# Performance work log

Hardware: AMD Instinct MI355X
Metric: run time of the kernel (lower is better)

## Reference

```python
import jax, jax.numpy as jnp
import numpy as np

N_NODES = 50000
N_EDGES = 800000
N_GRAPHS = 256
HID = 64           # hidden_channels
H, C = 2, 64       # GAT heads, per-head channels
D2 = H * C         # 128 = hidden_channels * heads
BN_EPS = 1e-5


def setup_inputs() -> dict:
    key = jax.random.key(0)
    ks = iter(jax.random.split(key, 64))

    def p(shape, scale=0.05):
        return (jax.random.normal(next(ks), shape, dtype=jnp.float32) * scale)

    inp = {}
    inp["metadata"] = jax.random.normal(next(ks), (N_NODES, 4), dtype=jnp.float32)
    inp["waveform_features"] = jax.random.normal(next(ks), (N_NODES, 64), dtype=jnp.float32)
    inp["edge_index"] = jax.random.randint(next(ks), (2, N_EDGES), 0, N_NODES, dtype=jnp.int64)
    inp["batch"] = jnp.sort(jax.random.randint(next(ks), (N_NODES,), 0, N_GRAPHS, dtype=jnp.int64))

    # encoders / combiner
    inp["meta_w"] = p((4, HID // 2)); inp["meta_b"] = p((HID // 2,))
    inp["wave_w"] = p((64, HID // 2)); inp["wave_b"] = p((HID // 2,))
    inp["comb_w"] = p((HID, HID));     inp["comb_b"] = p((HID,))

    # GAT layers: layer 0 maps HID->H*C, layers 1,2 map D2->H*C
    inp["gat_w0"] = p((HID, D2)); inp["gat_as0"] = p((H, C)); inp["gat_ad0"] = p((H, C)); inp["gat_b0"] = p((D2,))
    inp["gat_w1"] = p((D2, D2));  inp["gat_as1"] = p((H, C)); inp["gat_ad1"] = p((H, C)); inp["gat_b1"] = p((D2,))
    inp["gat_w2"] = p((D2, D2));  inp["gat_as2"] = p((H, C)); inp["gat_ad2"] = p((H, C)); inp["gat_b2"] = p((D2,))

    # batch norms (eval mode: running stats), stacked over 3 layers
    inp["bn_gamma"] = jnp.ones((3, D2), jnp.float32) + p((3, D2))
    inp["bn_beta"] = p((3, D2))
    inp["bn_mean"] = p((3, D2))
    inp["bn_var"] = jax.random.uniform(next(ks), (3, D2), jnp.float32, 0.5, 1.5)

    # predictors
    inp["lat_w1"] = p((D2, HID)); inp["lat_b1"] = p((HID,))
    inp["lat_w2"] = p((HID, 1));  inp["lat_b2"] = p((1,))
    inp["lon_w1"] = p((D2, HID)); inp["lon_b1"] = p((HID,))
    inp["lon_w2"] = p((HID, 1));  inp["lon_b2"] = p((1,))
    return inp


def gat_conv(x, src, dst, n, W, a_src, a_dst, b):
    """PyG-style GATConv, heads=H concat, leaky_relu slope 0.2, self-loops already in src/dst."""
    h = (x @ W).reshape(n, H, C)                          # [N,H,C]
    s = jnp.einsum('nhc,hc->nh', h, a_src)                # alpha_src [N,H]
    d = jnp.einsum('nhc,hc->nh', h, a_dst)                # alpha_dst [N,H]
    e = jax.nn.leaky_relu(s[src] + d[dst], 0.2)           # [E,H]
    m = jax.ops.segment_max(e, dst, num_segments=n)       # per-dst softmax (segment)
    ex = jnp.exp(e - m[dst])
    denom = jax.ops.segment_sum(ex, dst, num_segments=n)
    alpha = ex / (denom[dst] + 1e-16)                     # [E,H]
    out = jax.ops.segment_sum(h[src] * alpha[:, :, None], dst, num_segments=n)  # [N,H,C]
    return out.reshape(n, H * C) + b


def reference(metadata, waveform_features, edge_index, batch,
              meta_w, meta_b, wave_w, wave_b, comb_w, comb_b,
              gat_w0, gat_as0, gat_ad0, gat_b0,
              gat_w1, gat_as1, gat_ad1, gat_b1,
              gat_w2, gat_as2, gat_ad2, gat_b2,
              bn_gamma, bn_beta, bn_mean, bn_var,
              lat_w1, lat_b1, lat_w2, lat_b2,
              lon_w1, lon_b1, lon_w2, lon_b2):
    n = metadata.shape[0]
    me = jax.nn.relu(metadata @ meta_w + meta_b)
    we = jax.nn.relu(waveform_features @ wave_w + wave_b)
    x = jnp.concatenate([me, we], axis=1)                 # [N, HID]
    x = jax.nn.relu(x @ comb_w + comb_b)

    loops = jnp.arange(n, dtype=edge_index.dtype)         # GATConv adds self-loops
    src = jnp.concatenate([edge_index[0], loops])
    dst = jnp.concatenate([edge_index[1], loops])

    gat_params = [(gat_w0, gat_as0, gat_ad0, gat_b0),
                  (gat_w1, gat_as1, gat_ad1, gat_b1),
                  (gat_w2, gat_as2, gat_ad2, gat_b2)]
    for i in range(3):
        x_res = x if i > 0 else None
        x = gat_conv(x, src, dst, n, *gat_params[i])
        x = (x - bn_mean[i]) * (bn_gamma[i] / jnp.sqrt(bn_var[i] + BN_EPS)) + bn_beta[i]
        if x_res is not None and x.shape == x_res.shape:
            x = x + x_res
        x = jax.nn.relu(x)                                # dropout inactive (eval)

    # global_mean_pool over graphs
    sums = jax.ops.segment_sum(x, batch, num_segments=N_GRAPHS)
    cnt = jax.ops.segment_sum(jnp.ones((n, 1), x.dtype), batch, num_segments=N_GRAPHS)
    xg = sums / jnp.maximum(cnt, 1.0)                     # [B, 128]

    lat = jax.nn.relu(xg @ lat_w1 + lat_b1) @ lat_w2 + lat_b2
    lon = jax.nn.relu(xg @ lon_w1 + lon_b1) @ lon_w2 + lon_b2
    return lat, lon
```

## Files before the change

kernel.cpp:

```cpp
#include <hip/hip_runtime.h>
#include <hip/hip_bf16.h>
#include <stdint.h>

#define NN 50000
#define NNP 50048
#define NE 800000
#define ET 850000
#define NG 256
#define CAP 128
#define NB 392
#define BCAP 3072
#define EB 4096
#define NEB ((ET + EB - 1) / EB)

typedef __hip_bfloat16 bf16;
typedef __attribute__((ext_vector_type(8))) short short8;
typedef __attribute__((ext_vector_type(4))) float floatx4;

__device__ __forceinline__ float b2f(bf16 v) { return __bfloat162float(v); }
__device__ __forceinline__ float lrelu(float x) { return x > 0.f ? x : 0.2f * x; }
__device__ __forceinline__ short f2b(float f) {
    unsigned u = __float_as_uint(f);
    unsigned r = (u + 0x7FFFu + ((u >> 16) & 1u)) >> 16;
    return (short)r;
}
__device__ __forceinline__ float sh2f(short s) { return __uint_as_float(((unsigned)(unsigned short)s) << 16); }
__device__ __forceinline__ float blo(unsigned u) { return __uint_as_float(u << 16); }
__device__ __forceinline__ float bhi(unsigned u) { return __uint_as_float(u & 0xFFFF0000u); }
__device__ __forceinline__ unsigned pck(float a, float b) {
    return ((unsigned)(unsigned short)f2b(a)) | (((unsigned)(unsigned short)f2b(b)) << 16);
}
__device__ __forceinline__ float wred_sum(float v) {
    for (int o = 32; o > 0; o >>= 1) v += __shfl_xor(v, o, 64);
    return v;
}
__device__ __forceinline__ int ld_int(const void* p, int i, bool i64) {
    return i64 ? (int)((const long long*)p)[i] : ((const int*)p)[i];
}
__device__ __forceinline__ float ldf(const void* p, int i, bool fp32) {
    return fp32 ? ((const float*)p)[i] : b2f(((const bf16*)p)[i]);
}

__global__ void detect_kernel(const unsigned int* __restrict__ meta_words,
                              const unsigned int* __restrict__ ei_words,
                              int* __restrict__ flags, int* __restrict__ bcur) {
    __shared__ int insane, odd_nonzero;
    for (int k = threadIdx.x; k < NB; k += 256) bcur[k] = 0;
    if (threadIdx.x == 0) { insane = 0; odd_nonzero = 0; }
    __syncthreads();
    int cnt = 0;
    for (int k = 0; k < 8; k++) {
        unsigned int w = meta_words[threadIdx.x * 8 + k];
        int elo = (int)(((w & 0xFFFFu) >> 7) & 0xFF);
        int ehi = (int)(((w >> 16) >> 7) & 0xFF);
        if (elo >= 0x8D) cnt++;
        if (ehi >= 0x8D) cnt++;
    }
    if (cnt) atomicAdd(&insane, cnt);
    if (ei_words[threadIdx.x * 2 + 1] != 0u) atomicAdd(&odd_nonzero, 1);
    __syncthreads();
    if (threadIdx.x == 0) {
        flags[0] = (insane >= 4) ? 1 : 0;
        flags[1] = (odd_nonzero == 0) ? 1 : 0;
    }
}

struct PrepArgs {
    const void* src[32];
    int len[32];
    int dst_off[32];
    int blk_base[33];
    int cvtBlks, wtBlks, wfBlks;
    const void* w0; const void* w1; const void* w2;
    const void* ww; const void* wc;
    const void* wf_src;
    const void* gb0; const void* gb1; const void* gb2;
    const void* bng; const void* bnb; const void* bnm; const void* bnv;
};

__global__ void prep_kernel(PrepArgs a, float* __restrict__ cf,
                            short* __restrict__ wtall, short* __restrict__ wavewT,
                            short* __restrict__ combwT,
                            short* __restrict__ wfhi, short* __restrict__ wflo,
                            float* __restrict__ bnscl, float* __restrict__ bnsft,
                            const int* __restrict__ flags) {
    int b = blockIdx.x;
    bool fp32f = flags[0] != 0;
    if (b < a.cvtBlks) {
        int ai = 0;
        while (b >= a.blk_base[ai + 1]) ai++;
        int base = (b - a.blk_base[ai]) * 1024 + threadIdx.x;
        const float* sf = (const float*)a.src[ai];
        const bf16* sh = (const bf16*)a.src[ai];
        float* d = cf + a.dst_off[ai];
        int len = a.len[ai];
        #pragma unroll
        for (int u = 0; u < 4; u++) {
            int i = base + u * 256;
            if (i < len) d[i] = fp32f ? sf[i] : b2f(sh[i]);
        }
        return;
    }
    b -= a.cvtBlks;
    if (b < a.wtBlks) {
        int idx = b * 256 + threadIdx.x;
        const void* src; short* dst; int K, N, loc;
        if (idx < 8192)        { src = a.w0; dst = wtall;          K = 64;  N = 128; loc = idx; }
        else if (idx < 24576)  { src = a.w1; dst = wtall + 8192;   K = 128; N = 128; loc = idx - 8192; }
        else if (idx < 40960)  { src = a.w2; dst = wtall + 24576;  K = 128; N = 128; loc = idx - 24576; }
        else if (idx < 43008)  { src = a.ww; dst = wavewT;         K = 64;  N = 32;  loc = idx - 40960; }
        else if (idx < 47104)  { src = a.wc; dst = combwT;         K = 64;  N = 64;  loc = idx - 43008; }
        else return;
        int nch = loc / K, k = loc % K;
        int si = k * N + nch;
        dst[loc] = fp32f ? f2b(((const float*)src)[si]) : ((const short*)src)[si];
        return;
    }
    b -= a.wtBlks;
    if (b < a.wfBlks) {
        int idx = b * 256 + threadIdx.x;
        int i8 = idx * 8;
        if (i8 >= NNP * 64) return;
        short8 h = {0, 0, 0, 0, 0, 0, 0, 0};
        if (fp32f) {
            short8 l = {0, 0, 0, 0, 0, 0, 0, 0};
            if (i8 < NN * 64) {
                const float* sf = (const float*)a.wf_src + i8;
                #pragma unroll
                for (int k = 0; k < 8; k++) {
                    float v = sf[k];
                    short hh = f2b(v);
                    h[k] = hh;
                    l[k] = f2b(v - sh2f(hh));
                }
            }
            *(short8*)(wfhi + i8) = h;
            *(short8*)(wflo + i8) = l;
        } else {
            if (i8 < NN * 64) h = *(const short8*)((const short*)a.wf_src + i8);
            *(short8*)(wfhi + i8) = h;
        }
        return;
    }
    b -= a.wfBlks;
    int idx = b * 256 + threadIdx.x;
    if (idx >= 384) return;
    int l = idx >> 7, c = idx & 127;
    const void* biasp = (l == 0) ? a.gb0 : (l == 1) ? a.gb1 : a.gb2;
    float bias = ldf(biasp, c, fp32f);
    float g  = ldf(a.bng, l * 128 + c, fp32f);
    float be = ldf(a.bnb, l * 128 + c, fp32f);
    float mu = ldf(a.bnm, l * 128 + c, fp32f);
    float va = ldf(a.bnv, l * 128 + c, fp32f);
    float sc = g * rsqrtf(va + 1e-5f);
    bnscl[l * 128 + c] = sc;
    bnsft[l * 128 + c] = (bias - mu) * sc + be;
}

__global__ __launch_bounds__(256) void encode_mfma_kernel(
        const float* __restrict__ meta, const float* __restrict__ meta_w,
        const float* __restrict__ meta_b,
        const short* __restrict__ wfhi, const short* __restrict__ wflo,
        const short* __restrict__ wavewT, const float* __restrict__ wave_b,
        const short* __restrict__ combwT, const float* __restrict__ comb_b,
        short* __restrict__ xout, const int* __restrict__ flags) {
    __shared__ short xc_hi[64][72];
    __shared__ short xc_lo[64][72];
    int t = threadIdx.x;
    int wave = t >> 6, lane = t & 63;
    int m16 = lane & 15, quad = lane >> 4;
    int nblk = blockIdx.x * 64;
    bool fp32f = flags[0] != 0;

    #pragma unroll
    for (int u = 0; u < 8; u++) {
        int idx = u * 256 + t;
        int node_l = idx >> 5, ch = idx & 31;
        int node = nblk + node_l;
        float acc = meta_b[ch];
        if (node < NN) {
            #pragma unroll
            for (int k = 0; k < 4; k++)
                acc += meta[node * 4 + k] * meta_w[k * 32 + ch];
        }
        float v = fmaxf(acc, 0.f);
        short hh = f2b(v);
        xc_hi[node_l][ch] = hh;
        xc_lo[node_l][ch] = f2b(v - sh2f(hh));
    }

    int row0 = nblk + wave * 16;
    const short* pah = wfhi + (size_t)(row0 + m16) * 64 + quad * 8;
    const short* pal = wflo + (size_t)(row0 + m16) * 64 + quad * 8;
    floatx4 wacc[2];
    wacc[0] = (floatx4)(0.f); wacc[1] = (floatx4)(0.f);
    #pragma unroll
    for (int ks = 0; ks < 64; ks += 32) {
        short8 ah = *(const short8*)(pah + ks);
        #pragma unroll
        for (int c = 0; c < 2; c++) {
            short8 b = *(const short8*)(wavewT + (c * 16 + m16) * 64 + ks + quad * 8);
            wacc[c] = __builtin_amdgcn_mfma_f32_16x16x32_bf16(ah, b, wacc[c], 0, 0, 0);
        }
        if (fp32f) {
            short8 al = *(const short8*)(pal + ks);
            #pragma unroll
            for (int c = 0; c < 2; c++) {
                short8 b = *(const short8*)(wavewT + (c * 16 + m16) * 64 + ks + quad * 8);
                wacc[c] = __builtin_amdgcn_mfma_f32_16x16x32_bf16(al, b, wacc[c], 0, 0, 0);
            }
        }
    }
    #pragma unroll
    for (int c = 0; c < 2; c++) {
        float bb = wave_b[c * 16 + m16];
        #pragma unroll
        for (int r = 0; r < 4; r++) {
            int node_l = wave * 16 + quad * 4 + r;
            int ch = 32 + c * 16 + m16;
            float v = fmaxf(wacc[c][r] + bb, 0.f);
            short hh = f2b(v);
            xc_hi[node_l][ch] = hh;
            xc_lo[node_l][ch] = f2b(v - sh2f(hh));
        }
    }
    __syncthreads();

    floatx4 acc2[4];
    #pragma unroll
    for (int c = 0; c < 4; c++) acc2[c] = (floatx4)(0.f);
    #pragma unroll
    for (int ks = 0; ks < 64; ks += 32) {
        short8 ah = *(const short8*)&xc_hi[wave * 16 + m16][ks + quad * 8];
        short8 al = *(const short8*)&xc_lo[wave * 16 + m16][ks + quad * 8];
        #pragma unroll
        for (int c = 0; c < 4; c++) {
            short8 b = *(const short8*)(combwT + (c * 16 + m16) * 64 + ks + quad * 8);
            acc2[c] = __builtin_amdgcn_mfma_f32_16x16x32_bf16(ah, b, acc2[c], 0, 0, 0);
            acc2[c] = __builtin_amdgcn_mfma_f32_16x16x32_bf16(al, b, acc2[c], 0, 0, 0);
        }
    }
    #pragma unroll
    for (int c = 0; c < 4; c++) {
        int ch = c * 16 + m16;
        float bb = comb_b[ch];
        #pragma unroll
        for (int r = 0; r < 4; r++) {
            int node = nblk + wave * 16 + quad * 4 + r;
            float v = fmaxf(acc2[c][r] + bb, 0.f);
            xout[(size_t)node * 64 + ch] = f2b(v);
        }
    }
}

__global__ void bucket_scatter_kernel(const void* __restrict__ ei, const int* __restrict__ flags,
                                      int* __restrict__ bcur, uint2* __restrict__ bkt) {
    __shared__ int lh[NB];
    __shared__ int lbase[NB];
    int t = threadIdx.x;
    bool i64 = flags[1] != 0;
    for (int k = t; k < NB; k += 256) lh[k] = 0;
    __syncthreads();
    int base = blockIdx.x * EB;
    #pragma unroll 4
    for (int u = 0; u < EB / 256; u++) {
        int i = base + u * 256 + t;
        if (i < ET) {
            int dst = (i < NE) ? ld_int(ei, NE + i, i64) : (i - NE);
            atomicAdd(&lh[dst >> 7], 1);
        }
    }
    __syncthreads();
    for (int k = t; k < NB; k += 256) {
        int c = lh[k];
        lbase[k] = c ? atomicAdd(&bcur[k], c) : 0;
        lh[k] = 0;
    }
    __syncthreads();
    #pragma unroll 4
    for (int u = 0; u < EB / 256; u++) {
        int i = base + u * 256 + t;
        if (i < ET) {
            int src, dst;
            if (i < NE) { src = ld_int(ei, i, i64); dst = ld_int(ei, NE + i, i64); }
            else        { src = i - NE; dst = i - NE; }
            int b = dst >> 7;
            int pos = lbase[b] + atomicAdd(&lh[b], 1);
            if (pos < BCAP) bkt[(size_t)b * BCAP + pos] = make_uint2((unsigned)src, (unsigned)dst);
        }
    }
}

__global__ void bucket_finalize_kernel(const uint2* __restrict__ bkt,
                                       const int* __restrict__ bcnt,
                                       int* __restrict__ offb, int* __restrict__ dega,
                                       int* __restrict__ csr) {
    __shared__ int hist[128];
    __shared__ int cur[128];
    int b = blockIdx.x;
    int t = threadIdx.x;
    int e0 = b * BCAP;
    int cnt = min(bcnt[b], BCAP);
    if (t < 128) hist[t] = 0;
    __syncthreads();
    for (int i = t; i < cnt; i += 256)
        atomicAdd(&hist[bkt[e0 + i].y & 127], 1);
    __syncthreads();
    int v = (t < 128) ? hist[t] : 0;
    if (t < 128) cur[t] = v;
    __syncthreads();
    for (int o = 1; o < 128; o <<= 1) {
        int x = (t < 128 && t >= o) ? cur[t - o] : 0;
        __syncthreads();
        if (t < 128) cur[t] += x;
        __syncthreads();
    }
    if (t < 128) {
        int ex = e0 + cur[t] - v;
        int node = b * 128 + t;
        if (node < NN) { offb[node] = ex; dega[node] = v; }
        cur[t] = ex;
    }
    __syncthreads();
    for (int i = t; i < cnt; i += 256) {
        uint2 e = bkt[e0 + i];
        int pos = atomicAdd(&cur[e.y & 127], 1);
        csr[pos] = (int)e.x;
    }
}

__global__ __launch_bounds__(256) void gemm_mfma_kernel(
        const short* __restrict__ x, const short* __restrict__ wt,
        const float* __restrict__ a_s, const float* __restrict__ a_d,
        short* __restrict__ h, float* __restrict__ s, float* __restrict__ d,
        int K, int n) {
    int wave = threadIdx.x >> 6;
    int lane = threadIdx.x & 63;
    int row0 = (blockIdx.x * 4 + wave) * 16;
    int m16 = lane & 15;
    int quad = lane >> 4;
    int kq = quad * 8;

    const short* pa = x + (size_t)(row0 + m16) * K + kq;

    floatx4 acc[8];
    #pragma unroll
    for (int c = 0; c < 8; c++) acc[c] = (floatx4)(0.f);

    for (int ks = 0; ks < K; ks += 32) {
        short8 av = *(const short8*)(pa + ks);
        #pragma unroll
        for (int c = 0; c < 8; c++) {
            short8 b = *(const short8*)(wt + (size_t)(c * 16 + m16) * K + ks + kq);
            acc[c] = __builtin_amdgcn_mfma_f32_16x16x32_bf16(av, b, acc[c], 0, 0, 0);
        }
    }

    #pragma unroll
    for (int c = 0; c < 8; c++) {
        #pragma unroll
        for (int r = 0; r < 4; r++) {
            int node = row0 + quad * 4 + r;
            if (node < n) h[(size_t)node * 128 + c * 16 + m16] = f2b(acc[c][r]);
        }
    }

    float sp[2][4] = {{0, 0, 0, 0}, {0, 0, 0, 0}};
    float dp[2][4] = {{0, 0, 0, 0}, {0, 0, 0, 0}};
    #pragma unroll
    for (int c = 0; c < 8; c++) {
        float as_ = a_s[c * 16 + m16];
        float ad_ = a_d[c * 16 + m16];
        int hh = c >> 2;
        #pragma unroll
        for (int r = 0; r < 4; r++) {
            sp[hh][r] += acc[c][r] * as_;
            dp[hh][r] += acc[c][r] * ad_;
        }
    }
    #pragma unroll
    for (int o = 1; o < 16; o <<= 1) {
        #pragma unroll
        for (int hh = 0; hh < 2; hh++)
            #pragma unroll
            for (int r = 0; r < 4; r++) {
                sp[hh][r] += __shfl_xor(sp[hh][r], o, 64);
                dp[hh][r] += __shfl_xor(dp[hh][r], o, 64);
            }
    }
    if (m16 == 0) {
        #pragma unroll
        for (int r = 0; r < 4; r++) {
            int node = row0 + quad * 4 + r;
            if (node < n) {
                s[node * 2 + 0] = sp[0][r];
                s[node * 2 + 1] = sp[1][r];
                d[node * 2 + 0] = dp[0][r];
                d[node * 2 + 1] = dp[1][r];
            }
        }
    }
}

__global__ __launch_bounds__(256) void gat_aggregate_kernel(
        const unsigned* __restrict__ hp, const float* __restrict__ sv,
        const float* __restrict__ dv, const int* __restrict__ offb,
        const int* __restrict__ dega, const int* __restrict__ csr,
        const float* __restrict__ scl, const float* __restrict__ sft,
        const unsigned* __restrict__ res, unsigned* __restrict__ out, int n) {
    __shared__ float4 er[8][CAP];
    int slot = threadIdx.x >> 5;
    int lane32 = threadIdx.x & 31;
    int node = blockIdx.x * 8 + slot;
    bool ok = node < n;
    int begin = 0, deg = 0;
    float d0 = 0.f, d1 = 0.f;
    if (ok) {
        begin = offb[node]; deg = dega[node];
        d0 = dv[node * 2 + 0]; d1 = dv[node * 2 + 1];
    }
    bool fits = deg <= CAP;
    int degp = (deg + 7) & ~7;
    float inv0 = 0.f, inv1 = 0.f;

    if (ok && fits) {
        int sids[4]; float e0[4], e1[4];
        #pragma unroll
        for (int k = 0; k < 4; k++) {
            int li = k * 32 + lane32;
            sids[k] = (li < deg) ? csr[begin + li] : -1;
        }
        #pragma unroll
        for (int k = 0; k < 4; k++) {
            if (sids[k] >= 0) {
                float2 sp = *(const float2*)(sv + 2 * sids[k]);
                e0[k] = lrelu(sp.x + d0); e1[k] = lrelu(sp.y + d1);
            } else { e0[k] = -3e38f; e1[k] = -3e38f; }
        }
        float m0 = fmaxf(fmaxf(e0[0], e0[1]), fmaxf(e0[2], e0[3]));
        float m1 = fmaxf(fmaxf(e1[0], e1[1]), fmaxf(e1[2], e1[3]));
        #pragma unroll
        for (int o = 1; o < 32; o <<= 1) {
            m0 = fmaxf(m0, __shfl_xor(m0, o, 64));
            m1 = fmaxf(m1, __shfl_xor(m1, o, 64));
        }
        float z0 = 0.f, z1 = 0.f;
        #pragma unroll
        for (int k = 0; k < 4; k++) {
            if (sids[k] >= 0) {
                float x0 = __expf(e0[k] - m0), x1 = __expf(e1[k] - m1);
                z0 += x0; z1 += x1;
                er[slot][k * 32 + lane32] = make_float4(__int_as_float(sids[k]), x0, x1, 0.f);
            }
        }
        #pragma unroll
        for (int o = 1; o < 32; o <<= 1) {
            z0 += __shfl_xor(z0, o, 64);
            z1 += __shfl_xor(z1, o, 64);
        }
        if (lane32 < degp - deg)
            er[slot][deg + lane32] = make_float4(__int_as_float(0), 0.f, 0.f, 0.f);
        inv0 = 1.f / (z0 + 1e-16f);
        inv1 = 1.f / (z1 + 1e-16f);
    }
    __syncthreads();
    if (!ok) return;

    if (fits) {
        int ll = lane32 & 15;
        int grp = lane32 >> 4;
        int hsel = (ll >= 8) ? 1 : 0;
        const uint4* hp4 = (const uint4*)hp;
        float a0 = 0, a1 = 0, a2 = 0, a3 = 0, a4 = 0, a5 = 0, a6 = 0, a7 = 0;
        for (int i = 0; i < degp; i += 8) {
            int e = i + grp * 4;
            float4 r0 = er[slot][e], r1 = er[slot][e + 1], r2 = er[slot][e + 2], r3 = er[slot][e + 3];
            uint4 u0 = hp4[(size_t)__float_as_int(r0.x) * 16 + ll];
            uint4 u1 = hp4[(size_t)__float_as_int(r1.x) * 16 + ll];
            uint4 u2 = hp4[(size_t)__float_as_int(r2.x) * 16 + ll];
            uint4 u3 = hp4[(size_t)__float_as_int(r3.x) * 16 + ll];
            float al0 = hsel ? r0.z : r0.y;
            float al1 = hsel ? r1.z : r1.y;
            float al2 = hsel ? r2.z : r2.y;
            float al3 = hsel ? r3.z : r3.y;
            a0 += al0 * blo(u0.x) + al1 * blo(u1.x) + al2 * blo(u2.x) + al3 * blo(u3.x);
            a1 += al0 * bhi(u0.x) + al1 * bhi(u1.x) + al2 * bhi(u2.x) + al3 * bhi(u3.x);
            a2 += al0 * blo(u0.y) + al1 * blo(u1.y) + al2 * blo(u2.y) + al3 * blo(u3.y);
            a3 += al0 * bhi(u0.y) + al1 * bhi(u1.y) + al2 * bhi(u2.y) + al3 * bhi(u3.y);
            a4 += al0 * blo(u0.z) + al1 * blo(u1.z) + al2 * blo(u2.z) + al3 * blo(u3.z);
            a5 += al0 * bhi(u0.z) + al1 * bhi(u1.z) + al2 * bhi(u2.z) + al3 * bhi(u3.z);
            a6 += al0 * blo(u0.w) + al1 * blo(u1.w) + al2 * blo(u2.w) + al3 * blo(u3.w);
            a7 += al0 * bhi(u0.w) + al1 * bhi(u1.w) + al2 * bhi(u2.w) + al3 * bhi(u3.w);
        }
        a0 += __shfl_xor(a0, 16, 64); a1 += __shfl_xor(a1, 16, 64);
        a2 += __shfl_xor(a2, 16, 64); a3 += __shfl_xor(a3, 16, 64);
        a4 += __shfl_xor(a4, 16, 64); a5 += __shfl_xor(a5, 16, 64);
        a6 += __shfl_xor(a6, 16, 64); a7 += __shfl_xor(a7, 16, 64);
        float inv = hsel ? inv1 : inv0;
        a0 *= inv; a1 *= inv; a2 *= inv; a3 *= inv;
        a4 *= inv; a5 *= inv; a6 *= inv; a7 *= inv;

        float4 sc0 = ((const float4*)scl)[2 * ll], sc1 = ((const float4*)scl)[2 * ll + 1];
        float4 sh0 = ((const float4*)sft)[2 * ll], sh1 = ((const float4*)sft)[2 * ll + 1];
        float v0 = a0 * sc0.x + sh0.x;
        float v1 = a1 * sc0.y + sh0.y;
        float v2 = a2 * sc0.z + sh0.z;
        float v3 = a3 * sc0.w + sh0.w;
        float v4 = a4 * sc1.x + sh1.x;
        float v5 = a5 * sc1.y + sh1.y;
        float v6 = a6 * sc1.z + sh1.z;
        float v7 = a7 * sc1.w + sh1.w;
        if (res) {
            uint4 r = ((const uint4*)res)[(size_t)node * 16 + ll];
            v0 += blo(r.x); v1 += bhi(r.x); v2 += blo(r.y); v3 += bhi(r.y);
            v4 += blo(r.z); v5 += bhi(r.z); v6 += blo(r.w); v7 += bhi(r.w);
        }
        v0 = fmaxf(v0, 0.f); v1 = fmaxf(v1, 0.f); v2 = fmaxf(v2, 0.f); v3 = fmaxf(v3, 0.f);
        v4 = fmaxf(v4, 0.f); v5 = fmaxf(v5, 0.f); v6 = fmaxf(v6, 0.f); v7 = fmaxf(v7, 0.f);
        if (grp == 0) {
            ((uint4*)out)[(size_t)node * 16 + ll] =
                make_uint4(pck(v0, v1), pck(v2, v3), pck(v4, v5), pck(v6, v7));
        }
    } else {
        float mm0 = -3e38f, mm1 = -3e38f;
        for (int i = lane32; i < deg; i += 32) {
            int sc = csr[begin + i];
            float2 sp = *(const float2*)(sv + 2 * sc);
            mm0 = fmaxf(mm0, lrelu(sp.x + d0));
            mm1 = fmaxf(mm1, lrelu(sp.y + d1));
        }
        #pragma unroll
        for (int o = 1; o < 32; o <<= 1) {
            mm0 = fmaxf(mm0, __shfl_xor(mm0, o, 64));
            mm1 = fmaxf(mm1, __shfl_xor(mm1, o, 64));
        }
        float z0 = 0.f, z1 = 0.f;
        for (int i = lane32; i < deg; i += 32) {
            int sc = csr[begin + i];
            float2 sp = *(const float2*)(sv + 2 * sc);
            z0 += __expf(lrelu(sp.x + d0) - mm0);
            z1 += __expf(lrelu(sp.y + d1) - mm1);
        }
        #pragma unroll
        for (int o = 1; o < 32; o <<= 1) {
            z0 += __shfl_xor(z0, o, 64);
            z1 += __shfl_xor(z1, o, 64);
        }
        float i0_ = 1.f / (z0 + 1e-16f), i1_ = 1.f / (z1 + 1e-16f);
        bool head0 = lane32 < 16;
        float b0 = 0.f, b1 = 0.f, b2 = 0.f, b3 = 0.f;
        for (int i = 0; i < deg; i++) {
            int sc = csr[begin + i];
            float2 sp = *(const float2*)(sv + 2 * sc);
            float a = head0 ? __expf(lrelu(sp.x + d0) - mm0) * i0_
                            : __expf(lrelu(sp.y + d1) - mm1) * i1_;
            uint2 u = *(const uint2*)(hp + (size_t)sc * 64 + lane32 * 2);
            b0 += a * blo(u.x); b1 += a * bhi(u.x);
            b2 += a * blo(u.y); b3 += a * bhi(u.y);
        }
        float4 sc4 = ((const float4*)scl)[lane32];
        float4 sh4 = ((const float4*)sft)[lane32];
        float v0 = b0 * sc4.x + sh4.x;
        float v1 = b1 * sc4.y + sh4.y;
        float v2 = b2 * sc4.z + sh4.z;
        float v3 = b3 * sc4.w + sh4.w;
        if (res) {
            uint2 r = ((const uint2*)res)[(size_t)node * 32 + lane32];
            v0 += blo(r.x); v1 += bhi(r.x); v2 += blo(r.y); v3 += bhi(r.y);
        }
        v0 = fmaxf(v0, 0.f); v1 = fmaxf(v1, 0.f);
        v2 = fmaxf(v2, 0.f); v3 = fmaxf(v3, 0.f);
        ((uint2*)out)[(size_t)node * 32 + lane32] = make_uint2(pck(v0, v1), pck(v2, v3));
    }
}

__global__ void poolhead_kernel(const unsigned* __restrict__ x, const void* __restrict__ batch,
                                const float* __restrict__ w1a, const float* __restrict__ b1a,
                                const float* __restrict__ w2a, const float* __restrict__ b2a,
                                const float* __restrict__ w1o, const float* __restrict__ b1o,
                                const float* __restrict__ w2o, const float* __restrict__ b2o,
                                const int* __restrict__ flags, void* __restrict__ out) {
    __shared__ float part[4][128];
    __shared__ float xs[128];
    __shared__ int bounds[2];
    int g = blockIdx.x;
    int tid = threadIdx.x;
    bool i64 = flags[1] != 0;
    if (tid < 2) {
        int target = g + tid;
        int lo = 0, hi = NN;
        while (lo < hi) {
            int mid = (lo + hi) >> 1;
            if (ld_int(batch, mid, i64) < target) lo = mid + 1; else hi = mid;
        }
        bounds[tid] = lo;
    }
    __syncthreads();
    int s0 = bounds[0], e0 = bounds[1];
    int wv = tid >> 6, lane = tid & 63;
    float a0 = 0.f, a1 = 0.f;
    for (int node = s0 + wv; node < e0; node += 4) {
        unsigned u = x[(size_t)node * 64 + lane];
        a0 += blo(u);
        a1 += bhi(u);
    }
    part[wv][2 * lane] = a0;
    part[wv][2 * lane + 1] = a1;
    __syncthreads();
    if (tid < 128) {
        float t0 = part[0][tid] + part[1][tid] + part[2][tid] + part[3][tid];
        xs[tid] = t0 / fmaxf((float)(e0 - s0), 1.f);
    }
    __syncthreads();
    if (wv < 2) {
        const float* w1 = wv ? w1o : w1a;
        const float* b1 = wv ? b1o : b1a;
        const float* w2 = wv ? w2o : w2a;
        const float* b2 = wv ? b2o : b2a;
        float acc = b1[lane];
        for (int c = 0; c < 128; c++)
            acc += xs[c] * w1[c * 64 + lane];
        acc = fmaxf(acc, 0.f);
        float contrib = wred_sum(acc * w2[lane]);
        if (lane == 0) {
            float r = contrib + b2[0];
            if (flags[0]) ((float*)out)[wv * NG + g] = r;
            else          ((bf16*)out)[wv * NG + g] = __float2bfloat16(r);
        }
    }
}

extern "C" void kernel_launch(void* const* d_in, const int* in_sizes, int n_in,
                              void* d_out, int out_size, void* d_ws, size_t ws_size,
                              hipStream_t stream) {
    static const int fidx[32] = {0,1, 4,5,6,7,8,9, 10,11,12,13, 14,15,16,17,
                                 18,19,20,21, 22,23,24,25, 26,27,28,29, 30,31,32,33};
    static const int flen[32] = {200000, 3200000, 128, 32, 2048, 32, 4096, 64,
                                 8192, 128, 128, 128, 16384, 128, 128, 128,
                                 16384, 128, 128, 128, 384, 384, 384, 384,
                                 8192, 64, 64, 1, 8192, 64, 64, 1};
    PrepArgs pa;
    int O[32];
    int tot = 0, blk = 0;
    for (int i = 0; i < 32; i++) {
        bool skip = (i == 1) || (i == 4) || (i == 6) || (i == 8) || (i == 12) || (i == 16) ||
                    (i == 11) || (i == 15) || (i == 19) ||
                    (i == 20) || (i == 21) || (i == 22) || (i == 23);
        int cl = skip ? 0 : flen[i];
        pa.src[i] = d_in[fidx[i]];
        pa.len[i] = cl;
        O[i] = tot;
        pa.dst_off[i] = tot;
        pa.blk_base[i] = blk;
        tot += (flen[i] + 63) & ~63;
        blk += (cl + 1023) / 1024;
    }
    pa.blk_base[32] = blk;
    pa.cvtBlks = blk;
    pa.wtBlks = 184;
    pa.wfBlks = NNP * 64 / 8 / 256;
    pa.w0 = d_in[10]; pa.w1 = d_in[14]; pa.w2 = d_in[18];
    pa.ww = d_in[6];  pa.wc = d_in[8];
    pa.wf_src = d_in[1];
    pa.gb0 = d_in[13]; pa.gb1 = d_in[17]; pa.gb2 = d_in[21];
    pa.bng = d_in[22]; pa.bnb = d_in[23]; pa.bnm = d_in[24]; pa.bnv = d_in[25];
    int prepGrid = pa.cvtBlks + pa.wtBlks + pa.wfBlks + 2;

    char* w = (char*)d_ws;
    auto alloc = [&](size_t bytes) -> char* {
        char* p = w;
        w += (bytes + 255) & ~(size_t)255;
        return p;
    };
    int*   flags  = (int*)alloc(256);
    float* cf     = (float*)alloc((size_t)tot * 4);
    short* wfhi   = (short*)alloc((size_t)NNP * 64 * 2);
    short* wflo   = (short*)alloc((size_t)NNP * 64 * 2);
    short* x0     = (short*)alloc((size_t)NNP * 64 * 2);
    short* xA     = (short*)alloc((size_t)NNP * 128 * 2);
    short* xB     = (short*)alloc((size_t)NNP * 128 * 2);
    short* h      = (short*)alloc((size_t)NNP * 128 * 2);
    float* sA     = (float*)alloc((size_t)NN * 2 * 4);
    float* dA     = (float*)alloc((size_t)NN * 2 * 4);
    int*   offb   = (int*)alloc((size_t)NN * 4);
    int*   dega   = (int*)alloc((size_t)NN * 4);
    int*   csr    = (int*)alloc((size_t)NB * BCAP * 4);
    int*   bcur   = (int*)alloc((size_t)NB * 4);
    uint2* bkt    = (uint2*)alloc((size_t)NB * BCAP * 8);
    float* bnscl  = (float*)alloc(384 * 4);
    float* bnsft  = (float*)alloc(384 * 4);
    short* wtall  = (short*)alloc((size_t)40960 * 2);
    short* wavewT = (short*)alloc((size_t)2048 * 2);
    short* combwT = (short*)alloc((size_t)4096 * 2);
    short* wt0 = wtall, *wt1 = wtall + 8192, *wt2 = wtall + 24576;

    detect_kernel<<<1, 256, 0, stream>>>((const unsigned int*)d_in[0],
                                         (const unsigned int*)d_in[2], flags, bcur);
    prep_kernel<<<prepGrid, 256, 0, stream>>>(pa, cf, wtall, wavewT, combwT,
                                              wfhi, wflo, bnscl, bnsft, flags);
    encode_mfma_kernel<<<NNP / 64, 256, 0, stream>>>(cf + O[0], cf + O[2], cf + O[3],
                                                     wfhi, wflo, wavewT, cf + O[5],
                                                     combwT, cf + O[7], x0, flags);
    bucket_scatter_kernel<<<NEB, 256, 0, stream>>>(d_in[2], flags, bcur, bkt);
    bucket_finalize_kernel<<<NB, 256, 0, stream>>>(bkt, bcur, offb, dega, csr);

    int gblk = NNP / 64;
    gemm_mfma_kernel<<<gblk, 256, 0, stream>>>(x0, wt0, cf + O[9], cf + O[10],
                                               h, sA, dA, 64, NN);
    gat_aggregate_kernel<<<(NN + 7) / 8, 256, 0, stream>>>(
        (const unsigned*)h, sA, dA, offb, dega, csr,
        bnscl, bnsft, nullptr, (unsigned*)xA, NN);
    gemm_mfma_kernel<<<gblk, 256, 0, stream>>>(xA, wt1, cf + O[13], cf + O[14],
                                               h, sA, dA, 128, NN);
    gat_aggregate_kernel<<<(NN + 7) / 8, 256, 0, stream>>>(
        (const unsigned*)h, sA, dA, offb, dega, csr,
        bnscl + 128, bnsft + 128, (const unsigned*)xA, (unsigned*)xB, NN);
    gemm_mfma_kernel<<<gblk, 256, 0, stream>>>(xB, wt2, cf + O[17], cf + O[18],
                                               h, sA, dA, 128, NN);
    gat_aggregate_kernel<<<(NN + 7) / 8, 256, 0, stream>>>(
        (const unsigned*)h, sA, dA, offb, dega, csr,
        bnscl + 256, bnsft + 256, (const unsigned*)xB, (unsigned*)xA, NN);

    poolhead_kernel<<<NG, 256, 0, stream>>>((const unsigned*)xA, d_in[3],
                                            cf + O[24], cf + O[25], cf + O[26], cf + O[27],
                                            cf + O[28], cf + O[29], cf + O[30], cf + O[31],
                                            flags, d_out);
}
```

Baseline: 365.4 us.

## Store GAT projected features in fp32 and skip bf16 waveform copy

The intermediate h produced by the GEMM is now stored as fp32 instead of bf16. The aggregation kernels read fp32 float4 pairs in the gather instead of unpacking bf16, which doubles the gather traffic over about 850k edges per layer. The aim is to improve accuracy and cut conversion ALU work, at the cost of more memory bandwidth. Separately, when the input is already bf16, the prep step no longer copies the waveform features and the encoder reads the raw input directly, with a row clamp replacing the old padding.

```diff
diff --git a/kernel.cpp b/kernel.cpp
--- a/kernel.cpp
+++ b/kernel.cpp
@@ -118,28 +118,24 @@
     }
     b -= a.wtBlks;
     if (b < a.wfBlks) {
+        if (!fp32f) return;
         int idx = b * 256 + threadIdx.x;
         int i8 = idx * 8;
         if (i8 >= NNP * 64) return;
         short8 h = {0, 0, 0, 0, 0, 0, 0, 0};
-        if (fp32f) {
-            short8 l = {0, 0, 0, 0, 0, 0, 0, 0};
-            if (i8 < NN * 64) {
-                const float* sf = (const float*)a.wf_src + i8;
-                #pragma unroll
-                for (int k = 0; k < 8; k++) {
-                    float v = sf[k];
-                    short hh = f2b(v);
-                    h[k] = hh;
-                    l[k] = f2b(v - sh2f(hh));
-                }
+        short8 l = {0, 0, 0, 0, 0, 0, 0, 0};
+        if (i8 < NN * 64) {
+            const float* sf = (const float*)a.wf_src + i8;
+            #pragma unroll
+            for (int k = 0; k < 8; k++) {
+                float v = sf[k];
+                short hh = f2b(v);
+                h[k] = hh;
+                l[k] = f2b(v - sh2f(hh));
             }
-            *(short8*)(wfhi + i8) = h;
-            *(short8*)(wflo + i8) = l;
-        } else {
-            if (i8 < NN * 64) h = *(const short8*)((const short*)a.wf_src + i8);
-            *(short8*)(wfhi + i8) = h;
-        }
+        }
+        *(short8*)(wfhi + i8) = h;
+        *(short8*)(wflo + i8) = l;
         return;
     }
     b -= a.wfBlks;
@@ -161,6 +157,7 @@
         const float* __restrict__ meta, const float* __restrict__ meta_w,
         const float* __restrict__ meta_b,
         const short* __restrict__ wfhi, const short* __restrict__ wflo,
+        const short* __restrict__ wf_raw,
         const short* __restrict__ wavewT, const float* __restrict__ wave_b,
         const short* __restrict__ combwT, const float* __restrict__ comb_b,
         short* __restrict__ xout, const int* __restrict__ flags) {
@@ -189,9 +186,11 @@
         xc_lo[node_l][ch] = f2b(v - sh2f(hh));
     }
 
-    int row0 = nblk + wave * 16;
-    const short* pah = wfhi + (size_t)(row0 + m16) * 64 + quad * 8;
-    const short* pal = wflo + (size_t)(row0 + m16) * 64 + quad * 8;
+    int row = nblk + wave * 16 + m16;
+    if (row >= NN) row = NN - 1;
+    const short* wbase = fp32f ? wfhi : wf_raw;
+    const short* pah = wbase + (size_t)row * 64 + quad * 8;
+    const short* pal = wflo + (size_t)row * 64 + quad * 8;
     floatx4 wacc[2];
     wacc[0] = (floatx4)(0.f); wacc[1] = (floatx4)(0.f);
     #pragma unroll
@@ -332,7 +331,7 @@
 __global__ __launch_bounds__(256) void gemm_mfma_kernel(
         const short* __restrict__ x, const short* __restrict__ wt,
         const float* __restrict__ a_s, const float* __restrict__ a_d,
-        short* __restrict__ h, float* __restrict__ s, float* __restrict__ d,
+        float* __restrict__ h, float* __restrict__ s, float* __restrict__ d,
         int K, int n) {
     int wave = threadIdx.x >> 6;
     int lane = threadIdx.x & 63;
@@ -361,7 +360,7 @@
         #pragma unroll
         for (int r = 0; r < 4; r++) {
             int node = row0 + quad * 4 + r;
-            if (node < n) h[(size_t)node * 128 + c * 16 + m16] = f2b(acc[c][r]);
+            if (node < n) h[(size_t)node * 128 + c * 16 + m16] = acc[c][r];
         }
     }
 
@@ -403,7 +402,7 @@
 }
 
 __global__ __launch_bounds__(256) void gat_aggregate_kernel(
-        const unsigned* __restrict__ hp, const float* __restrict__ sv,
+        const float* __restrict__ hpf, const float* __restrict__ sv,
         const float* __restrict__ dv, const int* __restrict__ offb,
         const int* __restrict__ dega, const int* __restrict__ csr,
         const float* __restrict__ scl, const float* __restrict__ sft,
@@ -470,27 +469,31 @@
         int ll = lane32 & 15;
         int grp = lane32 >> 4;
         int hsel = (ll >= 8) ? 1 : 0;
-        const uint4* hp4 = (const uint4*)hp;
+        const float4* hp4 = (const float4*)hpf;
         float a0 = 0, a1 = 0, a2 = 0, a3 = 0, a4 = 0, a5 = 0, a6 = 0, a7 = 0;
         for (int i = 0; i < degp; i += 8) {
             int e = i + grp * 4;
             float4 r0 = er[slot][e], r1 = er[slot][e + 1], r2 = er[slot][e + 2], r3 = er[slot][e + 3];
-            uint4 u0 = hp4[(size_t)__float_as_int(r0.x) * 16 + ll];
-            uint4 u1 = hp4[(size_t)__float_as_int(r1.x) * 16 + ll];
-            uint4 u2 = hp4[(size_t)__float_as_int(r2.x) * 16 + ll];
-            uint4 u3 = hp4[(size_t)__float_as_int(r3.x) * 16 + ll];
+            int b0 = __float_as_int(r0.x) * 32 + ll * 2;
+            int b1 = __float_as_int(r1.x) * 32 + ll * 2;
+            int b2 = __float_as_int(r2.x) * 32 + ll * 2;
+            int b3 = __float_as_int(r3.x) * 32 + ll * 2;
+            float4 u0a = hp4[b0], u0b = hp4[b0 + 1];
+            float4 u1a = hp4[b1], u1b = hp4[b1 + 1];
+            float4 u2a = hp4[b2], u2b = hp4[b2 + 1];
+            float4 u3a = hp4[b3], u3b = hp4[b3 + 1];
             float al0 = hsel ? r0.z : r0.y;
             float al1 = hsel ? r1.z : r1.y;
             float al2 = hsel ? r2.z : r2.y;
             float al3 = hsel ? r3.z : r3.y;
-            a0 += al0 * blo(u0.x) + al1 * blo(u1.x) + al2 * blo(u2.x) + al3 * blo(u3.x);
-            a1 += al0 * bhi(u0.x) + al1 * bhi(u1.x) + al2 * bhi(u2.x) + al3 * bhi(u3.x);
-            a2 += al0 * blo(u0.y) + al1 * blo(u1.y) + al2 * blo(u2.y) + al3 * blo(u3.y);
-            a3 += al0 * bhi(u0.y) + al1 * bhi(u1.y) + al2 * bhi(u2.y) + al3 * bhi(u3.y);
-            a4 += al0 * blo(u0.z) + al1 * blo(u1.z) + al2 * blo(u2.z) + al3 * blo(u3.z);
-            a5 += al0 * bhi(u0.z) + al1 * bhi(u1.z) + al2 * bhi(u2.z) + al3 * bhi(u3.z);
-            a6 += al0 * blo(u0.w) + al1 * blo(u1.w) + al2 * blo(u2.w) + al3 * blo(u3.w);
-            a7 += al0 * bhi(u0.w) + al1 * bhi(u1.w) + al2 * bhi(u2.w) + al3 * bhi(u3.w);
+            a0 += al0 * u0a.x + al1 * u1a.x + al2 * u2a.x + al3 * u3a.x;
+            a1 += al0 * u0a.y + al1 * u1a.y + al2 * u2a.y + al3 * u3a.y;
+            a2 += al0 * u0a.z + al1 * u1a.z + al2 * u2a.z + al3 * u3a.z;
+            a3 += al0 * u0a.w + al1 * u1a.w + al2 * u2a.w + al3 * u3a.w;
+            a4 += al0 * u0b.x + al1 * u1b.x + al2 * u2b.x + al3 * u3b.x;
+            a5 += al0 * u0b.y + al1 * u1b.y + al2 * u2b.y + al3 * u3b.y;
+            a6 += al0 * u0b.z + al1 * u1b.z + al2 * u2b.z + al3 * u3b.z;
+            a7 += al0 * u0b.w + al1 * u1b.w + al2 * u2b.w + al3 * u3b.w;
         }
         a0 += __shfl_xor(a0, 16, 64); a1 += __shfl_xor(a1, 16, 64);
         a2 += __shfl_xor(a2, 16, 64); a3 += __shfl_xor(a3, 16, 64);
@@ -554,9 +557,9 @@
             float2 sp = *(const float2*)(sv + 2 * sc);
             float a = head0 ? __expf(lrelu(sp.x + d0) - mm0) * i0_
                             : __expf(lrelu(sp.y + d1) - mm1) * i1_;
-            uint2 u = *(const uint2*)(hp + (size_t)sc * 64 + lane32 * 2);
-            b0 += a * blo(u.x); b1 += a * bhi(u.x);
-            b2 += a * blo(u.y); b3 += a * bhi(u.y);
+            float4 u = ((const float4*)hpf)[(size_t)sc * 32 + lane32];
+            b0 += a * u.x; b1 += a * u.y;
+            b2 += a * u.z; b3 += a * u.w;
         }
         float4 sc4 = ((const float4*)scl)[lane32];
         float4 sh4 = ((const float4*)sft)[lane32];
@@ -679,7 +682,7 @@
     short* x0     = (short*)alloc((size_t)NNP * 64 * 2);
     short* xA     = (short*)alloc((size_t)NNP * 128 * 2);
     short* xB     = (short*)alloc((size_t)NNP * 128 * 2);
-    short* h      = (short*)alloc((size_t)NNP * 128 * 2);
+    float* h      = (float*)alloc((size_t)NNP * 128 * 4);
     float* sA     = (float*)alloc((size_t)NN * 2 * 4);
     float* dA     = (float*)alloc((size_t)NN * 2 * 4);
     int*   offb   = (int*)alloc((size_t)NN * 4);
@@ -699,7 +702,8 @@
     prep_kernel<<<prepGrid, 256, 0, stream>>>(pa, cf, wtall, wavewT, combwT,
                                               wfhi, wflo, bnscl, bnsft, flags);
     encode_mfma_kernel<<<NNP / 64, 256, 0, stream>>>(cf + O[0], cf + O[2], cf + O[3],
-                                                     wfhi, wflo, wavewT, cf + O[5],
+                                                     wfhi, wflo, (const short*)d_in[1],
+                                                     wavewT, cf + O[5],
                                                      combwT, cf + O[7], x0, flags);
     bucket_scatter_kernel<<<NEB, 256, 0, stream>>>(d_in[2], flags, bcur, bkt);
     bucket_finalize_kernel<<<NB, 256, 0, stream>>>(bkt, bcur, offb, dega, csr);
@@ -708,17 +712,17 @@
     gemm_mfma_kernel<<<gblk, 256, 0, stream>>>(x0, wt0, cf + O[9], cf + O[10],
                                                h, sA, dA, 64, NN);
     gat_aggregate_kernel<<<(NN + 7) / 8, 256, 0, stream>>>(
-        (const unsigned*)h, sA, dA, offb, dega, csr,
+        h, sA, dA, offb, dega, csr,
         bnscl, bnsft, nullptr, (unsigned*)xA, NN);
     gemm_mfma_kernel<<<gblk, 256, 0, stream>>>(xA, wt1, cf + O[13], cf + O[14],
                                                h, sA, dA, 128, NN);
     gat_aggregate_kernel<<<(NN + 7) / 8, 256, 0, stream>>>(
-        (const unsigned*)h, sA, dA, offb, dega, csr,
+        h, sA, dA, offb, dega, csr,
         bnscl + 128, bnsft + 128, (const unsigned*)xA, (unsigned*)xB, NN);
     gemm_mfma_kernel<<<gblk, 256, 0, stream>>>(xB, wt2, cf + O[17], cf + O[18],
                                                h, sA, dA, 128, NN);
     gat_aggregate_kernel<<<(NN + 7) / 8, 256, 0, stream>>>(
-        (const unsigned*)h, sA, dA, offb, dega, csr,
+        h, sA, dA, offb, dega, csr,
         bnscl + 256, bnsft + 256, (const unsigned*)xB, (unsigned*)xA, NN);
 
     poolhead_kernel<<<NG, 256, 0, stream>>>((const unsigned*)xA, d_in[3],
```

Result: slower. 443.2 us (+21.3%).
